# Performance work log

Measured on AMD Instinct MI355X. Metric: run time of the kernel, lower is better.

The kernel has to match this reference:

```python
import jax, jax.numpy as jnp
import numpy as np

B, T, F = 32, 4096, 512
H = 512

def setup_inputs() -> dict:
    key = jax.random.key(0)
    k1, k2, k3, k4, k5 = jax.random.split(key, 5)
    enc = jax.random.normal(k1, (B, T, F), dtype=jnp.float32)
    dec = jax.random.normal(k2, (B, F), dtype=jnp.float32)
    # Dense kernels (no bias), scaled like Glorot-ish init
    W1 = jax.random.normal(k3, (F, H), dtype=jnp.float32) / np.sqrt(F)
    W2 = jax.random.normal(k4, (F, H), dtype=jnp.float32) / np.sqrt(F)
    V = jax.random.normal(k5, (H, 1), dtype=jnp.float32) / np.sqrt(H)
    return {"encoder_outputs": enc, "dec_output": dec, "W1": W1, "W2": W2, "V": V}

def reference(encoder_outputs, dec_output, W1, W2, V):
    # Bahdanau additive attention, fully vectorized over time_steps
    # (the original runs this step-by-step via K.rnn; state is unchanged,
    # so the computation is embarrassingly parallel over t).
    w1_e = jnp.einsum('btf,fh->bth', encoder_outputs, W1)   # [B,T,H]
    w2_d = jnp.einsum('bf,fh->bh', dec_output, W2)          # [B,H]
    scores = jnp.einsum('bth,h->bt', jnp.tanh(w1_e + w2_d[:, None, :]), V[:, 0])  # [B,T]
    return jax.nn.softmax(scores, axis=1)
```

## Files before the change

kernel.cpp:

```cpp
#include <hip/hip_runtime.h>
#include <hip/hip_bf16.h>

#define B_ 32
#define T_ 4096
#define F_ 512
#define H_ 512

typedef float floatx4 __attribute__((ext_vector_type(4)));
typedef short short8 __attribute__((ext_vector_type(8)));

__device__ __forceinline__ unsigned pack2_bf16(float a, float b) {
  unsigned ua = __float_as_uint(a);
  unsigned ub = __float_as_uint(b);
  ua = (ua + 0x7FFFu + ((ua >> 16) & 1u)) >> 16;
  ub = (ub + 0x7FFFu + ((ub >> 16) & 1u)) & 0xFFFF0000u;
  return ua | ub;
}

__device__ __forceinline__ unsigned short f2bf16(float a) {
  unsigned ua = __float_as_uint(a);
  return (unsigned short)((ua + 0x7FFFu + ((ua >> 16) & 1u)) >> 16);
}

__device__ __forceinline__ float tanh_fast(float x) {
  float e = __expf(2.0f * x);
  return 1.0f - __fdividef(2.0f, e + 1.0f);
}

__device__ __forceinline__ void async_load16(const void* g, void* l) {
  __builtin_amdgcn_global_load_lds(
      (const __attribute__((address_space(1))) void*)g,
      (__attribute__((address_space(3))) void*)l, 16, 0, 0);
}

__global__ void prep_w1t(const float* __restrict__ W1, unsigned short* __restrict__ W1T) {
  __shared__ float tile[32][33];
  const int tx = threadIdx.x, ty = threadIdx.y;
  const int f = blockIdx.y * 32 + ty;
  const int h = blockIdx.x * 32 + tx;
  tile[ty][tx] = W1[f * H_ + h];
  __syncthreads();
  const int ho = blockIdx.x * 32 + ty;
  const int fo = blockIdx.y * 32 + tx;
  W1T[ho * F_ + fo] = f2bf16(tile[tx][ty]);
}

__global__ __launch_bounds__(128) void prep_w2d(const float* __restrict__ dec,
                                                const float* __restrict__ W2,
                                                float* __restrict__ w2d) {
  const int b = blockIdx.x;
  const int h = blockIdx.y * 128 + threadIdx.x;
  float s0 = 0.f, s1 = 0.f, s2 = 0.f, s3 = 0.f;
  for (int f = 0; f < F_; f += 4) {
    s0 += dec[b * F_ + f + 0] * W2[(f + 0) * H_ + h];
    s1 += dec[b * F_ + f + 1] * W2[(f + 1) * H_ + h];
    s2 += dec[b * F_ + f + 2] * W2[(f + 2) * H_ + h];
    s3 += dec[b * F_ + f + 3] * W2[(f + 3) * H_ + h];
  }
  w2d[b * H_ + h] = (s0 + s1) + (s2 + s3);
}

__global__ __launch_bounds__(256, 3) void fused_score(
    const float* __restrict__ enc, const unsigned short* __restrict__ W1T,
    const float* __restrict__ w2d, const float* __restrict__ V,
    float* __restrict__ scores) {
  __shared__ __align__(16) unsigned short As[2][128 * 40];
  __shared__ __align__(16) unsigned short Bs[2][128 * 32];

  const int tid = threadIdx.x;
  const int bid = blockIdx.x;
  const int xcd = bid & 7;
  const int ii = bid >> 3;
  const int n_blk = ii & 3;
  const int m_blk = xcd + ((ii >> 2) << 3);
  const int lane = tid & 63;
  const int wave = tid >> 6;
  const int wm = wave >> 1;
  const int wn = wave & 1;
  const int quad = lane >> 4;
  const int l16 = lane & 15;

  const int arow = tid >> 2;
  const int acol = (tid & 3) * 8;
  const float* aptr = enc + (size_t)(m_blk * 128 + arow) * F_ + acol;

  const int nb0 = wave * 32;
  const int bl_n = lane >> 2;
  const int bl_c = (lane & 3) ^ (bl_n & 3);
  const unsigned short* bsrc0 =
      W1T + (size_t)(n_blk * 128 + nb0 + bl_n) * F_ + bl_c * 8;
  const unsigned short* bsrc1 = bsrc0 + 16 * F_;

  floatx4 acc[4][4];
#pragma unroll
  for (int i = 0; i < 4; i++)
#pragma unroll
    for (int j = 0; j < 4; j++) acc[i][j] = (floatx4){0.f, 0.f, 0.f, 0.f};

  float4 a_pre[4];

#pragma unroll
  for (int rr = 0; rr < 2; ++rr) {
    a_pre[rr * 2 + 0] = *(const float4*)(aptr + rr * 64 * F_ + 0);
    a_pre[rr * 2 + 1] = *(const float4*)(aptr + rr * 64 * F_ + 4);
  }
#pragma unroll
  for (int rr = 0; rr < 2; ++rr) {
    uint4 pk;
    pk.x = pack2_bf16(a_pre[rr * 2].x, a_pre[rr * 2].y);
    pk.y = pack2_bf16(a_pre[rr * 2].z, a_pre[rr * 2].w);
    pk.z = pack2_bf16(a_pre[rr * 2 + 1].x, a_pre[rr * 2 + 1].y);
    pk.w = pack2_bf16(a_pre[rr * 2 + 1].z, a_pre[rr * 2 + 1].w);
    *(uint4*)&As[0][(arow + rr * 64) * 40 + acol] = pk;
  }
  async_load16(bsrc0, &Bs[0][nb0 * 32]);
  async_load16(bsrc1, &Bs[0][(nb0 + 16) * 32]);
  __syncthreads();

  for (int ks = 0; ks < 16; ++ks) {
    const int cur = ks & 1;
    const int nxt = cur ^ 1;

    if (ks < 15) {
      const int k1 = (ks + 1) * 32;
#pragma unroll
      for (int rr = 0; rr < 2; ++rr) {
        a_pre[rr * 2 + 0] = *(const float4*)(aptr + rr * 64 * F_ + k1);
        a_pre[rr * 2 + 1] = *(const float4*)(aptr + rr * 64 * F_ + k1 + 4);
      }
      async_load16(bsrc0 + k1, &Bs[nxt][nb0 * 32]);
      async_load16(bsrc1 + k1, &Bs[nxt][(nb0 + 16) * 32]);
    }

    short8 af[4], bfr[4];
#pragma unroll
    for (int i = 0; i < 4; i++)
      af[i] = *(const short8*)&As[cur][(wm * 64 + i * 16 + l16) * 40 + quad * 8];
#pragma unroll
    for (int j = 0; j < 4; j++)
      bfr[j] = *(const short8*)&Bs[cur][(wn * 64 + j * 16 + l16) * 32 +
                                        ((quad ^ (l16 & 3)) * 8)];
#pragma unroll
    for (int i = 0; i < 4; i++)
#pragma unroll
      for (int j = 0; j < 4; j++)
        acc[i][j] = __builtin_amdgcn_mfma_f32_16x16x32_bf16(af[i], bfr[j], acc[i][j], 0, 0, 0);

    if (ks < 15) {
#pragma unroll
      for (int rr = 0; rr < 2; ++rr) {
        uint4 pk;
        pk.x = pack2_bf16(a_pre[rr * 2].x, a_pre[rr * 2].y);
        pk.y = pack2_bf16(a_pre[rr * 2].z, a_pre[rr * 2].w);
        pk.z = pack2_bf16(a_pre[rr * 2 + 1].x, a_pre[rr * 2 + 1].y);
        pk.w = pack2_bf16(a_pre[rr * 2 + 1].z, a_pre[rr * 2 + 1].w);
        *(uint4*)&As[nxt][(arow + rr * 64) * 40 + acol] = pk;
      }
    }
    __syncthreads();
  }

  const int b = m_blk >> 5;
  float w2v[4], vv[4];
#pragma unroll
  for (int j = 0; j < 4; j++) {
    const int h = n_blk * 128 + wn * 64 + j * 16 + l16;
    w2v[j] = w2d[b * H_ + h];
    vv[j] = V[h];
  }
  float rs[4][4];
#pragma unroll
  for (int i = 0; i < 4; i++)
#pragma unroll
    for (int r = 0; r < 4; r++) {
      float s = 0.f;
#pragma unroll
      for (int j = 0; j < 4; j++) s += tanh_fast(acc[i][j][r] + w2v[j]) * vv[j];
      rs[i][r] = s;
    }
#pragma unroll
  for (int i = 0; i < 4; i++)
#pragma unroll
    for (int r = 0; r < 4; r++) {
      float s = rs[i][r];
      s += __shfl_xor(s, 1, 16);
      s += __shfl_xor(s, 2, 16);
      s += __shfl_xor(s, 4, 16);
      s += __shfl_xor(s, 8, 16);
      rs[i][r] = s;
    }
  if (l16 == 0) {
#pragma unroll
    for (int i = 0; i < 4; i++)
#pragma unroll
      for (int r = 0; r < 4; r++)
        atomicAdd(&scores[m_blk * 128 + wm * 64 + i * 16 + quad * 4 + r], rs[i][r]);
  }
}

__global__ __launch_bounds__(256) void softmax_rows(const float* __restrict__ scores,
                                                    float* __restrict__ out) {
  const int b = blockIdx.x;
  const int tid = threadIdx.x;
  const int wave = tid >> 6;
  __shared__ float red[4];
  float v[16];
  float mx = -1e30f;
#pragma unroll
  for (int i = 0; i < 16; i++) {
    v[i] = scores[b * T_ + i * 256 + tid];
    mx = fmaxf(mx, v[i]);
  }
#pragma unroll
  for (int o = 32; o > 0; o >>= 1) mx = fmaxf(mx, __shfl_xor(mx, o, 64));
  if ((tid & 63) == 0) red[wave] = mx;
  __syncthreads();
  mx = fmaxf(fmaxf(red[0], red[1]), fmaxf(red[2], red[3]));
  __syncthreads();
  float sum = 0.f;
#pragma unroll
  for (int i = 0; i < 16; i++) {
    v[i] = __expf(v[i] - mx);
    sum += v[i];
  }
#pragma unroll
  for (int o = 32; o > 0; o >>= 1) sum += __shfl_xor(sum, o, 64);
  if ((tid & 63) == 0) red[wave] = sum;
  __syncthreads();
  sum = (red[0] + red[1]) + (red[2] + red[3]);
  const float inv = 1.0f / sum;
#pragma unroll
  for (int i = 0; i < 16; i++) out[b * T_ + i * 256 + tid] = v[i] * inv;
}

extern "C" void kernel_launch(void* const* d_in, const int* in_sizes, int n_in,
                              void* d_out, int out_size, void* d_ws, size_t ws_size,
                              hipStream_t stream) {
  const float* enc = (const float*)d_in[0];
  const float* dec = (const float*)d_in[1];
  const float* W1 = (const float*)d_in[2];
  const float* W2 = (const float*)d_in[3];
  const float* V = (const float*)d_in[4];
  float* out = (float*)d_out;

  char* ws = (char*)d_ws;
  float* scores = (float*)ws;
  unsigned short* W1T = (unsigned short*)(ws + 524288);
  float* w2d = (float*)(ws + 1048576);

  (void)in_sizes; (void)n_in; (void)out_size; (void)ws_size;

  hipMemsetAsync(scores, 0, B_ * T_ * sizeof(float), stream);
  prep_w1t<<<dim3(16, 16), dim3(32, 32), 0, stream>>>(W1, W1T);
  prep_w2d<<<dim3(32, 4), dim3(128), 0, stream>>>(dec, W2, w2d);
  fused_score<<<dim3(4096), dim3(256), 0, stream>>>(enc, W1T, w2d, V, scores);
  softmax_rows<<<dim3(32), dim3(256), 0, stream>>>(scores, out);
}
```

Before: 477.9 us.

## Pre-convert encoder outputs to bf16 and stream both GEMM operands via async LDS loads

Adds a kernel that converts the fp32 encoder tensor to bf16 in workspace. The score GEMM then loads both operands with direct global-to-LDS async copies and a swizzled layout, instead of register-staged fp32 loads plus in-loop packing. This removes conversion work and register pressure from the main loop, at the cost of an extra full pass that reads and writes the large input. The old fp32 kernel remains as a fallback when the workspace is too small.

Result: slower. 511.6 us (+7.1%).

```diff
diff --git a/kernel.cpp b/kernel.cpp
--- a/kernel.cpp
+++ b/kernel.cpp
@@ -31,6 +31,22 @@
   __builtin_amdgcn_global_load_lds(
       (const __attribute__((address_space(1))) void*)g,
       (__attribute__((address_space(3))) void*)l, 16, 0, 0);
+}
+
+__global__ __launch_bounds__(256) void prep_enc(const float* __restrict__ enc,
+                                                unsigned short* __restrict__ encb) {
+  const int base = blockIdx.x * 512 + threadIdx.x;
+  const float4* e4 = (const float4*)enc;
+  uint2* o2 = (uint2*)encb;
+  const float4 a = e4[base];
+  const float4 b = e4[base + 256];
+  uint2 pa, pb;
+  pa.x = pack2_bf16(a.x, a.y);
+  pa.y = pack2_bf16(a.z, a.w);
+  pb.x = pack2_bf16(b.x, b.y);
+  pb.y = pack2_bf16(b.z, b.w);
+  o2[base] = pa;
+  o2[base + 256] = pb;
 }
 
 __global__ void prep_w1t(const float* __restrict__ W1, unsigned short* __restrict__ W1T) {
@@ -60,11 +76,11 @@
   w2d[b * H_ + h] = (s0 + s1) + (s2 + s3);
 }
 
-__global__ __launch_bounds__(256, 3) void fused_score(
-    const float* __restrict__ enc, const unsigned short* __restrict__ W1T,
+__global__ __launch_bounds__(256) void fused_score_bf16(
+    const unsigned short* __restrict__ encb, const unsigned short* __restrict__ W1T,
     const float* __restrict__ w2d, const float* __restrict__ V,
     float* __restrict__ scores) {
-  __shared__ __align__(16) unsigned short As[2][128 * 40];
+  __shared__ __align__(16) unsigned short As[2][128 * 32];
   __shared__ __align__(16) unsigned short Bs[2][128 * 32];
 
   const int tid = threadIdx.x;
@@ -80,6 +96,115 @@
   const int quad = lane >> 4;
   const int l16 = lane & 15;
 
+  const int srow = lane >> 2;
+  const int schunk = (lane & 3) ^ ((srow + (srow >> 2)) & 3);
+  const unsigned short* asrc0 =
+      encb + (size_t)(m_blk * 128 + wave * 32 + srow) * F_ + schunk * 8;
+  const unsigned short* asrc1 = asrc0 + 16 * F_;
+  const unsigned short* bsrc0 =
+      W1T + (size_t)(n_blk * 128 + wave * 32 + srow) * F_ + schunk * 8;
+  const unsigned short* bsrc1 = bsrc0 + 16 * F_;
+  unsigned short* adst0[2] = {&As[0][wave * 1024], &As[1][wave * 1024]};
+  unsigned short* bdst0[2] = {&Bs[0][wave * 1024], &Bs[1][wave * 1024]};
+
+  floatx4 acc[4][4];
+#pragma unroll
+  for (int i = 0; i < 4; i++)
+#pragma unroll
+    for (int j = 0; j < 4; j++) acc[i][j] = (floatx4){0.f, 0.f, 0.f, 0.f};
+
+  const int fl = (l16 + (l16 >> 2)) & 3;
+  const int slot8 = (quad ^ fl) * 8;
+
+  async_load16(asrc0, adst0[0]);
+  async_load16(asrc1, adst0[0] + 512);
+  async_load16(bsrc0, bdst0[0]);
+  async_load16(bsrc1, bdst0[0] + 512);
+  __syncthreads();
+
+  for (int ks = 0; ks < 16; ++ks) {
+    const int cur = ks & 1;
+    const int nxt = cur ^ 1;
+    if (ks < 15) {
+      const int k1 = (ks + 1) * 32;
+      async_load16(asrc0 + k1, adst0[nxt]);
+      async_load16(asrc1 + k1, adst0[nxt] + 512);
+      async_load16(bsrc0 + k1, bdst0[nxt]);
+      async_load16(bsrc1 + k1, bdst0[nxt] + 512);
+    }
+    short8 af[4], bfr[4];
+#pragma unroll
+    for (int i = 0; i < 4; i++)
+      af[i] = *(const short8*)&As[cur][(wm * 64 + i * 16 + l16) * 32 + slot8];
+#pragma unroll
+    for (int j = 0; j < 4; j++)
+      bfr[j] = *(const short8*)&Bs[cur][(wn * 64 + j * 16 + l16) * 32 + slot8];
+#pragma unroll
+    for (int i = 0; i < 4; i++)
+#pragma unroll
+      for (int j = 0; j < 4; j++)
+        acc[i][j] = __builtin_amdgcn_mfma_f32_16x16x32_bf16(af[i], bfr[j], acc[i][j], 0, 0, 0);
+    __syncthreads();
+  }
+
+  const int b = m_blk >> 5;
+  float w2v[4], vv[4];
+#pragma unroll
+  for (int j = 0; j < 4; j++) {
+    const int h = n_blk * 128 + wn * 64 + j * 16 + l16;
+    w2v[j] = w2d[b * H_ + h];
+    vv[j] = V[h];
+  }
+  float rs[4][4];
+#pragma unroll
+  for (int i = 0; i < 4; i++)
+#pragma unroll
+    for (int r = 0; r < 4; r++) {
+      float s = 0.f;
+#pragma unroll
+      for (int j = 0; j < 4; j++) s += tanh_fast(acc[i][j][r] + w2v[j]) * vv[j];
+      rs[i][r] = s;
+    }
+#pragma unroll
+  for (int i = 0; i < 4; i++)
+#pragma unroll
+    for (int r = 0; r < 4; r++) {
+      float s = rs[i][r];
+      s += __shfl_xor(s, 1, 16);
+      s += __shfl_xor(s, 2, 16);
+      s += __shfl_xor(s, 4, 16);
+      s += __shfl_xor(s, 8, 16);
+      rs[i][r] = s;
+    }
+  if (l16 == 0) {
+#pragma unroll
+    for (int i = 0; i < 4; i++)
+#pragma unroll
+      for (int r = 0; r < 4; r++)
+        atomicAdd(&scores[m_blk * 128 + wm * 64 + i * 16 + quad * 4 + r], rs[i][r]);
+  }
+}
+
+__global__ __launch_bounds__(256, 3) void fused_score_f32(
+    const float* __restrict__ enc, const unsigned short* __restrict__ W1T,
+    const float* __restrict__ w2d, const float* __restrict__ V,
+    float* __restrict__ scores) {
+  __shared__ __align__(16) unsigned short As[2][128 * 40];
+  __shared__ __align__(16) unsigned short Bs[2][128 * 32];
+
+  const int tid = threadIdx.x;
+  const int bid = blockIdx.x;
+  const int xcd = bid & 7;
+  const int ii = bid >> 3;
+  const int n_blk = ii & 3;
+  const int m_blk = xcd + ((ii >> 2) << 3);
+  const int lane = tid & 63;
+  const int wave = tid >> 6;
+  const int wm = wave >> 1;
+  const int wn = wave & 1;
+  const int quad = lane >> 4;
+  const int l16 = lane & 15;
+
   const int arow = tid >> 2;
   const int acol = (tid & 3) * 8;
   const float* aptr = enc + (size_t)(m_blk * 128 + arow) * F_ + acol;
@@ -98,7 +223,6 @@
     for (int j = 0; j < 4; j++) acc[i][j] = (floatx4){0.f, 0.f, 0.f, 0.f};
 
   float4 a_pre[4];
-
 #pragma unroll
   for (int rr = 0; rr < 2; ++rr) {
     a_pre[rr * 2 + 0] = *(const float4*)(aptr + rr * 64 * F_ + 0);
@@ -120,7 +244,6 @@
   for (int ks = 0; ks < 16; ++ks) {
     const int cur = ks & 1;
     const int nxt = cur ^ 1;
-
     if (ks < 15) {
       const int k1 = (ks + 1) * 32;
 #pragma unroll
@@ -131,7 +254,6 @@
       async_load16(bsrc0 + k1, &Bs[nxt][nb0 * 32]);
       async_load16(bsrc1 + k1, &Bs[nxt][(nb0 + 16) * 32]);
     }
-
     short8 af[4], bfr[4];
 #pragma unroll
     for (int i = 0; i < 4; i++)
@@ -145,7 +267,6 @@
 #pragma unroll
       for (int j = 0; j < 4; j++)
         acc[i][j] = __builtin_amdgcn_mfma_f32_16x16x32_bf16(af[i], bfr[j], acc[i][j], 0, 0, 0);
-
     if (ks < 15) {
 #pragma unroll
       for (int rr = 0; rr < 2; ++rr) {
@@ -247,12 +368,20 @@
   float* scores = (float*)ws;
   unsigned short* W1T = (unsigned short*)(ws + 524288);
   float* w2d = (float*)(ws + 1048576);
-
-  (void)in_sizes; (void)n_in; (void)out_size; (void)ws_size;
+  unsigned short* encb = (unsigned short*)(ws + 2097152);
+
+  (void)in_sizes; (void)n_in; (void)out_size;
+
+  const size_t need = 2097152ull + (size_t)B_ * T_ * F_ * 2ull;
 
   hipMemsetAsync(scores, 0, B_ * T_ * sizeof(float), stream);
   prep_w1t<<<dim3(16, 16), dim3(32, 32), 0, stream>>>(W1, W1T);
   prep_w2d<<<dim3(32, 4), dim3(128), 0, stream>>>(dec, W2, w2d);
-  fused_score<<<dim3(4096), dim3(256), 0, stream>>>(enc, W1T, w2d, V, scores);
+  if (ws_size >= need) {
+    prep_enc<<<dim3(32768), dim3(256), 0, stream>>>(enc, encb);
+    fused_score_bf16<<<dim3(4096), dim3(256), 0, stream>>>(encb, W1T, w2d, V, scores);
+  } else {
+    fused_score_f32<<<dim3(4096), dim3(256), 0, stream>>>(enc, W1T, w2d, V, scores);
+  }
   softmax_rows<<<dim3(32), dim3(256), 0, stream>>>(scores, out);
 }
```
